# Kernel optimization log

Hardware: AMD Instinct MI355X
Metric: run time of the kernel (lower is better)

Reference implementation:

```python
import jax, jax.numpy as jnp
import numpy as np

CHEB_K = 3  # from init_kwargs

def _layernorm(v, g, b, eps=1e-12):
    mu = jnp.mean(v, axis=-1, keepdims=True)
    var = jnp.var(v, axis=-1, keepdims=True)  # biased, matches torch LayerNorm
    return (v - mu) * jax.lax.rsqrt(var + eps) * g + b

def setup_inputs() -> dict:
    key = jax.random.key(0)
    ks = jax.random.split(key, 5)
    B, N, D_IN, D_OUT, E = 64, 2048, 64, 64, 16
    return {
        "x": jax.random.normal(ks[0], (B, N, D_IN), dtype=jnp.float32),
        "node_embeddings": jax.random.normal(ks[1], (N, E), dtype=jnp.float32),
        "time_embeddings": jax.random.normal(ks[2], (E,), dtype=jnp.float32),
        "weights_pool": jax.random.normal(ks[3], (E, CHEB_K, D_IN, D_OUT), dtype=jnp.float32) * 0.1,
        "bias_pool": jax.random.normal(ks[4], (E, D_OUT), dtype=jnp.float32) * 0.1,
        "ln_gamma": jnp.ones((E,), dtype=jnp.float32),
        "ln_beta": jnp.zeros((E,), dtype=jnp.float32),
    }

def reference(x, node_embeddings, time_embeddings, weights_pool, bias_pool, ln_gamma, ln_beta):
    N = node_embeddings.shape[0]
    # dropout in eval mode -> identity
    ne = _layernorm(node_embeddings + time_embeddings[None, :], ln_gamma, ln_beta)  # [N,E]
    supports0 = jax.nn.softmax(ne @ ne.T, axis=1)  # [N,N]
    support_set = [jnp.eye(N, dtype=x.dtype), supports0]
    for _ in range(2, CHEB_K):
        support_set.append(2.0 * supports0 @ support_set[-1] - support_set[-2])
    supports = jnp.stack(support_set, axis=0)  # [K,N,N]
    weights = jnp.einsum('nd,dkio->nkio', ne, weights_pool)  # [N,K,I,O]
    bias = ne @ bias_pool  # [N,O]
    x_g = jnp.einsum('knm,bmc->bnkc', supports, x)  # [B,N,K,I]
    return jnp.einsum('bnki,nkio->bno', x_g, weights) + bias  # [B,N,O]
```

## Files before the change

### kernel.cpp

```cpp
#include <hip/hip_runtime.h>
#include <stdint.h>

typedef unsigned short u16;
typedef __attribute__((ext_vector_type(8))) short   bf16x8;
typedef __attribute__((ext_vector_type(4))) float   f32x4;
typedef __attribute__((ext_vector_type(4))) u16     u16x4;
typedef __attribute__((ext_vector_type(8))) u16     u16x8;

#define NN 2048
#define BB 64
#define DD 64
#define XSTRIDE (NN*DD)

__device__ __forceinline__ float bf2f(u16 u) {
    union { unsigned int i; float f; } v; v.i = ((unsigned int)u) << 16; return v.f;
}
__device__ __forceinline__ u16 f2bf(float f) {
    union { float f; unsigned int i; } v; v.f = f;
    unsigned int u = v.i;
    return (u16)((u + 0x7fffu + ((u >> 16) & 1u)) >> 16);
}

typedef __attribute__((address_space(3))) unsigned int lds_u32_t;
typedef const __attribute__((address_space(1))) unsigned int g_u32_t;
__device__ __forceinline__ void gload_lds16(const void* g, void* l) {
    __builtin_amdgcn_global_load_lds((g_u32_t*)(uintptr_t)g, (lds_u32_t*)(uintptr_t)l, 16, 0, 0);
}

__global__ __launch_bounds__(256) void k_ln(const float* __restrict__ nodee,
                                            const float* __restrict__ timee,
                                            const float* __restrict__ gamma,
                                            const float* __restrict__ beta,
                                            float* __restrict__ ne,
                                            u16* __restrict__ neb) {
    int n = blockIdx.x * 256 + threadIdx.x;
    float v[16]; float mu = 0.f;
    const float4* p = (const float4*)(nodee + (long)n * 16);
#pragma unroll
    for (int i = 0; i < 4; i++) {
        float4 q = p[i];
        v[i*4+0]=q.x; v[i*4+1]=q.y; v[i*4+2]=q.z; v[i*4+3]=q.w;
    }
#pragma unroll
    for (int e = 0; e < 16; e++) { v[e] += timee[e]; mu += v[e]; }
    mu *= (1.f/16.f);
    float var = 0.f;
#pragma unroll
    for (int e = 0; e < 16; e++) { float d = v[e]-mu; var += d*d; }
    var *= (1.f/16.f);
    float rs = rsqrtf(var + 1e-12f);
    float4* o = (float4*)(ne + (long)n * 16);
    u16x8 nb[2];
#pragma unroll
    for (int i = 0; i < 4; i++) {
        float4 q;
        q.x = (v[i*4+0]-mu)*rs*gamma[i*4+0] + beta[i*4+0];
        q.y = (v[i*4+1]-mu)*rs*gamma[i*4+1] + beta[i*4+1];
        q.z = (v[i*4+2]-mu)*rs*gamma[i*4+2] + beta[i*4+2];
        q.w = (v[i*4+3]-mu)*rs*gamma[i*4+3] + beta[i*4+3];
        o[i] = q;
        nb[i>>1][(i&1)*4+0] = f2bf(q.x); nb[i>>1][(i&1)*4+1] = f2bf(q.y);
        nb[i>>1][(i&1)*4+2] = f2bf(q.z); nb[i>>1][(i&1)*4+3] = f2bf(q.w);
    }
    u16x8 z;
#pragma unroll
    for (int j = 0; j < 8; j++) z[j] = 0;
    u16x8* ob = (u16x8*)&neb[(long)n * 32];
    ob[0] = nb[0]; ob[1] = nb[1]; ob[2] = z; ob[3] = z;
}

__global__ __launch_bounds__(256) void k_wperm(const float* __restrict__ wp,
                                               u16* __restrict__ wpP) {
    int j = blockIdx.x * 256 + threadIdx.x;
    int o = j / 192, ki = j - o * 192;
    int src = ki * 64 + o;
    u16x8 ov[4];
#pragma unroll
    for (int e = 0; e < 16; e++) ov[e>>3][e&7] = f2bf(wp[(long)e*12288 + src]);
#pragma unroll
    for (int e = 0; e < 8; e++) { ov[2][e] = 0; ov[3][e] = 0; }
    u16x8* dst = (u16x8*)&wpP[(long)j * 32];
    dst[0]=ov[0]; dst[1]=ov[1]; dst[2]=ov[2]; dst[3]=ov[3];
}

__global__ __launch_bounds__(256) void k_softmax(const float* __restrict__ ne,
                                                 u16* __restrict__ S) {
    __shared__ float row[2048];
    __shared__ float red[8];
    int n = blockIdx.x, t = threadIdx.x;
    int wave = t >> 6, lane = t & 63;
    f32x4 nev[4];
#pragma unroll
    for (int i = 0; i < 4; i++) nev[i] = *(const f32x4*)&ne[n*16 + i*4];
    float lmax = -1e30f;
    for (int m = t; m < 2048; m += 256) {
        const f32x4* p = (const f32x4*)&ne[m*16];
        f32x4 d4 = nev[0]*p[0] + nev[1]*p[1] + nev[2]*p[2] + nev[3]*p[3];
        float d = d4[0]+d4[1]+d4[2]+d4[3];
        row[m] = d;
        lmax = fmaxf(lmax, d);
    }
#pragma unroll
    for (int off = 32; off > 0; off >>= 1) lmax = fmaxf(lmax, __shfl_xor(lmax, off));
    if (lane == 0) red[wave] = lmax;
    __syncthreads();
    float gmax = fmaxf(fmaxf(red[0], red[1]), fmaxf(red[2], red[3]));
    float lsum = 0.f;
    for (int m = t; m < 2048; m += 256) {
        float ev = __expf(row[m] - gmax);
        row[m] = ev;
        lsum += ev;
    }
#pragma unroll
    for (int off = 32; off > 0; off >>= 1) lsum += __shfl_xor(lsum, off);
    __syncthreads();
    if (lane == 0) red[wave] = lsum;
    __syncthreads();
    float inv = 1.f / (red[0]+red[1]+red[2]+red[3]);
    for (int m = t; m < 2048; m += 256)
        S[(long)n*2048 + m] = f2bf(row[m] * inv);
}

__global__ __launch_bounds__(256) void k_permute(const float* __restrict__ x,
                                                 u16* __restrict__ Xpt) {
    __shared__ u16 T[64][72];
    int bid = blockIdx.x;
    int b = bid >> 5, m0 = (bid & 31) * 64;
    int t = threadIdx.x;
#pragma unroll
    for (int it = 0; it < 4; it++) {
        int fi = it*256 + t;
        int row = fi >> 4, c4 = (fi & 15) * 4;
        float4 v = *(const float4*)&x[(long)b*XSTRIDE + (m0+row)*64 + c4];
        T[c4+0][row] = f2bf(v.x); T[c4+1][row] = f2bf(v.y);
        T[c4+2][row] = f2bf(v.z); T[c4+3][row] = f2bf(v.w);
    }
    __syncthreads();
#pragma unroll
    for (int it = 0; it < 2; it++) {
        int ch = it*256 + t;
        int c = ch >> 3, m8 = (ch & 7) * 8;
        u16x8 v = *(const u16x8*)&T[c][m8];
        *(u16x8*)&Xpt[(long)(b*64 + c)*2048 + m0 + m8] = v;
    }
}

__global__ __launch_bounds__(256) void k_gemm_bt(const u16* __restrict__ A,
                                                 const u16* __restrict__ Bt,
                                                 u16* __restrict__ C,
                                                 int M, int Ncols, int K) {
    __shared__ __align__(16) u16 As[128*32];
    __shared__ __align__(16) u16 Bs[128*32];
    const int t = threadIdx.x;
    const int wave = t >> 6, lane = t & 63;
    const int l15 = lane & 15, lhi = lane >> 4;
    const int m0 = blockIdx.y * 128;
    const int n0 = blockIdx.x * 128;
    const int wr = wave >> 1, wc = wave & 1;
    f32x4 acc[4][4] = {};
    const int srow = t >> 2;
    const int sk = (t & 3) * 8;
    const u16* gA = A + (long)(m0 + srow) * K + sk;
    const u16* gB = Bt + (long)(n0 + srow) * K + sk;
    const long half = (long)64 * K;
    u16* lA = As + wave * 512;
    u16* lB = Bs + wave * 512;
    const int aoff = (wr*64 + l15)*32 + lhi*8;
    const int boff = (wc*64 + l15)*32 + lhi*8;
    for (int k0 = 0; k0 < K; k0 += 32) {
        gload_lds16(gA + k0,        lA);
        gload_lds16(gA + k0 + half, lA + 2048);
        gload_lds16(gB + k0,        lB);
        gload_lds16(gB + k0 + half, lB + 2048);
        __syncthreads();
        bf16x8 af[4], bv[4];
#pragma unroll
        for (int m = 0; m < 4; m++) af[m] = *(const bf16x8*)&As[aoff + m*512];
#pragma unroll
        for (int q = 0; q < 4; q++) bv[q] = *(const bf16x8*)&Bs[boff + q*512];
#pragma unroll
        for (int m = 0; m < 4; m++)
#pragma unroll
            for (int q = 0; q < 4; q++)
                acc[m][q] = __builtin_amdgcn_mfma_f32_16x16x32_bf16(af[m], bv[q], acc[m][q], 0, 0, 0);
        __syncthreads();
    }
#pragma unroll
    for (int m = 0; m < 4; m++) {
        int row = m0 + wr*64 + m*16 + lhi*4;
#pragma unroll
        for (int q = 0; q < 4; q++) {
            int col = n0 + wc*64 + q*16 + l15;
#pragma unroll
            for (int r = 0; r < 4; r++)
                C[(long)(row + r) * Ncols + col] = f2bf(acc[m][q][r]);
        }
    }
}

__global__ __launch_bounds__(512, 2) void k_gemm_big(const u16* __restrict__ A,
                                                     const u16* __restrict__ Bt,
                                                     u16* __restrict__ C,
                                                     u16* __restrict__ Ct,
                                                     int M, int Ncols, int K) {
    __shared__ __align__(16) u16 LB[73728];
    const int t = threadIdx.x;
    const int wave = t >> 6, lane = t & 63;
    const int l15 = lane & 15, lhi = lane >> 4;
    const int nwg = gridDim.x * gridDim.y;
    const int wgid = blockIdx.y * gridDim.x + blockIdx.x;
    const int swz = (wgid & 7) * (nwg >> 3) + (wgid >> 3);
    const int by = swz / gridDim.x, bx = swz - by * gridDim.x;
    const int m0 = by * 128, n0 = bx * 256;
    const int wr = wave >> 2, wc = wave & 3;
    const int NT = K >> 6;
    f32x4 acc[4][4] = {};

    const int srow = t >> 3;
    const int sswz = ((t & 7) ^ (srow & 7)) * 8;
    const u16* gA0 = A  + (long)(m0 + srow) * K + sswz;
    const u16* gB0 = Bt + (long)(n0 + srow) * K + sswz;
    const long rP = (long)64 * K;
    const int ldsW = wave * 512;

    int curA = 0,     nxtA = 8192,  tgtA = 16384;
    int curB = 24576, nxtB = 40960, tgtB = 57344;

    gload_lds16(gA0,           &LB[curA + 0*4096 + ldsW]);
    gload_lds16(gA0 + rP,      &LB[curA + 1*4096 + ldsW]);
#pragma unroll
    for (int r = 0; r < 4; r++) gload_lds16(gB0 + r*rP,      &LB[curB + r*4096 + ldsW]);
    gload_lds16(gA0 + 64,      &LB[nxtA + 0*4096 + ldsW]);
    gload_lds16(gA0 + rP + 64, &LB[nxtA + 1*4096 + ldsW]);
#pragma unroll
    for (int r = 0; r < 4; r++) gload_lds16(gB0 + r*rP + 64, &LB[nxtB + r*4096 + ldsW]);
    asm volatile("s_waitcnt vmcnt(6)" ::: "memory");
    __builtin_amdgcn_s_barrier();
    asm volatile("" ::: "memory");

    const int rsw = l15 & 7;
    const int sw0 = (lhi ^ rsw) * 8;
    const int sw1 = ((4 + lhi) ^ rsw) * 8;
    const int abase = (wr*64 + l15) * 64;
    const int bbase = (wc*64 + l15) * 64;

#pragma unroll 1
    for (int tt = 0; tt < NT; tt++) {
        const bool stg = (tt + 2 < NT);
        const long ko2 = (long)((tt + 2) << 6);
        bf16x8 af0[4], af1[4], bv0[4], bv1[4];
#pragma unroll
        for (int m = 0; m < 4; m++) af0[m] = *(const bf16x8*)&LB[curA + abase + m*1024 + sw0];
        bv0[0] = *(const bf16x8*)&LB[curB + bbase + 0*1024 + sw0];
        bv0[1] = *(const bf16x8*)&LB[curB + bbase + 1*1024 + sw0];
        if (stg) {
            gload_lds16(gA0 + ko2,      &LB[tgtA + 0*4096 + ldsW]);
            gload_lds16(gA0 + rP + ko2, &LB[tgtA + 1*4096 + ldsW]);
        }
        __builtin_amdgcn_s_barrier();
        asm volatile("s_waitcnt lgkmcnt(0)" ::: "memory");
        __builtin_amdgcn_s_setprio(1);
#pragma unroll
        for (int m = 0; m < 4; m++)
#pragma unroll
            for (int q = 0; q < 2; q++)
                acc[m][q] = __builtin_amdgcn_mfma_f32_16x16x32_bf16(af0[m], bv0[q], acc[m][q], 0, 0, 0);
        __builtin_amdgcn_s_setprio(0);
        __builtin_amdgcn_s_barrier();
        bv0[2] = *(const bf16x8*)&LB[curB + bbase + 2*1024 + sw0];
        bv0[3] = *(const bf16x8*)&LB[curB + bbase + 3*1024 + sw0];
        if (stg) {
            gload_lds16(gB0 + ko2,      &LB[tgtB + 0*4096 + ldsW]);
            gload_lds16(gB0 + rP + ko2, &LB[tgtB + 1*4096 + ldsW]);
        }
        __builtin_amdgcn_s_barrier();
        asm volatile("s_waitcnt lgkmcnt(0)" ::: "memory");
        __builtin_amdgcn_s_setprio(1);
#pragma unroll
        for (int m = 0; m < 4; m++)
#pragma unroll
            for (int q = 2; q < 4; q++)
                acc[m][q] = __builtin_amdgcn_mfma_f32_16x16x32_bf16(af0[m], bv0[q], acc[m][q], 0, 0, 0);
        __builtin_amdgcn_s_setprio(0);
        __builtin_amdgcn_s_barrier();
#pragma unroll
        for (int m = 0; m < 4; m++) af1[m] = *(const bf16x8*)&LB[curA + abase + m*1024 + sw1];
        bv1[0] = *(const bf16x8*)&LB[curB + bbase + 0*1024 + sw1];
        bv1[1] = *(const bf16x8*)&LB[curB + bbase + 1*1024 + sw1];
        if (stg) {
            gload_lds16(gB0 + 2*rP + ko2, &LB[tgtB + 2*4096 + ldsW]);
            gload_lds16(gB0 + 3*rP + ko2, &LB[tgtB + 3*4096 + ldsW]);
        }
        __builtin_amdgcn_s_barrier();
        asm volatile("s_waitcnt lgkmcnt(0)" ::: "memory");
        __builtin_amdgcn_s_setprio(1);
#pragma unroll
        for (int m = 0; m < 4; m++)
#pragma unroll
            for (int q = 0; q < 2; q++)
                acc[m][q] = __builtin_amdgcn_mfma_f32_16x16x32_bf16(af1[m], bv1[q], acc[m][q], 0, 0, 0);
        __builtin_amdgcn_s_setprio(0);
        __builtin_amdgcn_s_barrier();
        bv1[2] = *(const bf16x8*)&LB[curB + bbase + 2*1024 + sw1];
        bv1[3] = *(const bf16x8*)&LB[curB + bbase + 3*1024 + sw1];
        __builtin_amdgcn_s_barrier();
        asm volatile("s_waitcnt lgkmcnt(0)" ::: "memory");
        __builtin_amdgcn_s_setprio(1);
#pragma unroll
        for (int m = 0; m < 4; m++)
#pragma unroll
            for (int q = 2; q < 4; q++)
                acc[m][q] = __builtin_amdgcn_mfma_f32_16x16x32_bf16(af1[m], bv1[q], acc[m][q], 0, 0, 0);
        __builtin_amdgcn_s_setprio(0);
        asm volatile("" ::: "memory");
        if (tt + 1 < NT) {
            if (stg) asm volatile("s_waitcnt vmcnt(6)" ::: "memory");
            else     asm volatile("s_waitcnt vmcnt(0)" ::: "memory");
            __builtin_amdgcn_s_barrier();
            asm volatile("" ::: "memory");
        }
        int ta = curA; curA = nxtA; nxtA = tgtA; tgtA = ta;
        int tb = curB; curB = nxtB; nxtB = tgtB; tgtB = tb;
    }
#pragma unroll
    for (int m = 0; m < 4; m++) {
        int row = m0 + wr*64 + m*16 + lhi*4;
#pragma unroll
        for (int q = 0; q < 4; q++) {
            int col = n0 + wc*64 + q*16 + l15;
#pragma unroll
            for (int r = 0; r < 4; r++)
                C[(long)(row + r) * Ncols + col] = f2bf(acc[m][q][r]);
        }
    }
    if (Ct != nullptr) {
        __syncthreads();
#pragma unroll
        for (int m = 0; m < 4; m++) {
            int rowb = wr*64 + m*16 + lhi*4;
#pragma unroll
            for (int q = 0; q < 4; q++) {
                int col = wc*64 + q*16 + l15;
                u16x4 p;
                p[0]=f2bf(acc[m][q][0]); p[1]=f2bf(acc[m][q][1]);
                p[2]=f2bf(acc[m][q][2]); p[3]=f2bf(acc[m][q][3]);
                *(u16x4*)&LB[col*136 + rowb] = p;
            }
        }
        __syncthreads();
        const int j16 = t >> 4, ch = (t & 15) * 8;
#pragma unroll
        for (int p = 0; p < 8; p++) {
            int j = p*32 + j16;
            u16x8 v = *(const u16x8*)&LB[j*136 + ch];
            *(u16x8*)&Ct[(long)(n0 + j)*M + m0 + ch] = v;
        }
    }
}

__global__ __launch_bounds__(256) void k_final(const float* __restrict__ x,
                                               const u16* __restrict__ Y1,
                                               const u16* __restrict__ Y2,
                                               const u16* __restrict__ Wt,
                                               const float* __restrict__ ne,
                                               const float* __restrict__ bp,
                                               float* __restrict__ out) {
    __shared__ __align__(16) u16 Al[64*200];
    __shared__ __align__(16) u16 Wl[64*200];
    __shared__ float biasl[64];
    int n = blockIdx.x;
    int t = threadIdx.x;
    int wave = t >> 6, lane = t & 63;
    int l15 = lane & 15, lhi = lane >> 4;
#pragma unroll
    for (int it = 0; it < 6; it++) {
        int ch = it*256 + t;
        int o = ch / 24, kl = (ch % 24) * 8;
        u16x8 v = *(const u16x8*)&Wt[(long)n*12288 + ch*8];
        *(u16x8*)&Wl[o*200 + kl] = v;
    }
    float xs[16];
#pragma unroll
    for (int it = 0; it < 4; it++) {
        int fi = it*256 + t;
        int b = fi >> 4, i4 = (fi & 15) * 4;
        float4 v = *(const float4*)&x[(long)b*XSTRIDE + n*64 + i4];
        xs[it*4+0]=v.x; xs[it*4+1]=v.y; xs[it*4+2]=v.z; xs[it*4+3]=v.w;
        u16x4 p; p[0]=f2bf(v.x); p[1]=f2bf(v.y); p[2]=f2bf(v.z); p[3]=f2bf(v.w);
        *(u16x4*)&Al[b*200 + i4] = p;
    }
#pragma unroll
    for (int it = 0; it < 2; it++) {
        int ch = it*256 + t;
        int b = ch >> 3, i8 = (ch & 7)*8;
        u16x8 v = *(const u16x8*)&Y1[(long)n*4096 + ch*8];
        *(u16x8*)&Al[b*200 + 64 + i8] = v;
    }
#pragma unroll
    for (int it = 0; it < 4; it++) {
        int fi = it*256 + t;
        int b = fi >> 4, i4 = (fi & 15)*4;
        u16x4 y = *(const u16x4*)&Y2[(long)n*4096 + fi*4];
        u16x4 p;
#pragma unroll
        for (int j = 0; j < 4; j++) p[j] = f2bf(2.f*bf2f(y[j]) - xs[it*4+j]);
        *(u16x4*)&Al[b*200 + 128 + i4] = p;
    }
    if (t < 64) {
        float s = 0.f;
#pragma unroll
        for (int e = 0; e < 16; e++) s += ne[n*16+e] * bp[e*64 + t];
        biasl[t] = s;
    }
    __syncthreads();
    f32x4 acc[4] = {};
#pragma unroll
    for (int kk = 0; kk < 6; kk++) {
        bf16x8 bv = *(const bf16x8*)&Wl[(wave*16 + l15)*200 + kk*32 + lhi*8];
#pragma unroll
        for (int m = 0; m < 4; m++) {
            bf16x8 av = *(const bf16x8*)&Al[(m*16 + l15)*200 + kk*32 + lhi*8];
            acc[m] = __builtin_amdgcn_mfma_f32_16x16x32_bf16(av, bv, acc[m], 0, 0, 0);
        }
    }
    int o = wave*16 + l15;
    float bias = biasl[o];
#pragma unroll
    for (int m = 0; m < 4; m++) {
        int brow = m*16 + lhi*4;
#pragma unroll
        for (int r = 0; r < 4; r++)
            out[(long)(brow + r)*XSTRIDE + n*64 + o] = acc[m][r] + bias;
    }
}

extern "C" void kernel_launch(void* const* d_in, const int* in_sizes, int n_in,
                              void* d_out, int out_size, void* d_ws, size_t ws_size,
                              hipStream_t stream) {
    const float* x     = (const float*)d_in[0];
    const float* nodee = (const float*)d_in[1];
    const float* timee = (const float*)d_in[2];
    const float* wp    = (const float*)d_in[3];
    const float* bp    = (const float*)d_in[4];
    const float* gamma = (const float*)d_in[5];
    const float* beta  = (const float*)d_in[6];
    float* out = (float*)d_out;

    char* ws = (char*)d_ws;
    float* ne  = (float*)(ws);
    u16* S     = (u16*)(ws + 131072);
    u16* Xpt   = (u16*)(ws + 8519680);
    u16* Y1    = (u16*)(ws + 25296896);
    u16* Y1t   = (u16*)(ws + 42074112);
    u16* Y2    = (u16*)(ws + 58851328);
    u16* Wt    = (u16*)(ws + 75628544);
    u16* neb   = (u16*)(ws + 58851328);
    u16* wpP   = (u16*)(ws + 58851328 + 131072);
    if (ws_size < (size_t)125960192) return;

    k_ln      <<<8,    256, 0, stream>>>(nodee, timee, gamma, beta, ne, neb);
    k_wperm   <<<48,   256, 0, stream>>>(wp, wpP);
    k_gemm_bt <<<dim3(96,16), 256, 0, stream>>>(neb, wpP, Wt, 2048, 12288, 32);
    k_softmax <<<2048, 256, 0, stream>>>(ne, S);
    k_permute <<<2048, 256, 0, stream>>>(x, Xpt);
    k_gemm_big<<<dim3(16,16), 512, 0, stream>>>(S, Xpt, Y1, Y1t, 2048, 4096, 2048);
    k_gemm_big<<<dim3(16,16), 512, 0, stream>>>(S, Y1t, Y2, (u16*)nullptr, 2048, 4096, 2048);
    k_final   <<<2048, 256, 0, stream>>>(x, Y1, Y2, Wt, ne, bp, out);
}
```

Baseline: 155.9 us.

## Drop intra-iteration barriers in big GEMM loop and lower occupancy target

Replaces the four-phase ping-pong schedule inside the big GEMM main loop (with barriers between each MFMA cluster) with two half-K phases that issue all LDS fragment loads and then 16 MFMAs, leaving a single barrier per iteration. Global-to-LDS prefetch issue is redistributed across the two halves. Launch bounds drop from 2 to 1 workgroups per CU, allowing more registers per thread but reducing cross-workgroup latency hiding. The intent is to cut barrier stalls, at the cost of occupancy and of less interleaving between LDS reads and MFMA.

Result: faster. 150.7 us (-3.4%).

```diff
diff --git a/kernel.cpp b/kernel.cpp
--- a/kernel.cpp
+++ b/kernel.cpp
@@ -198,7 +198,7 @@
     }
 }
 
-__global__ __launch_bounds__(512, 2) void k_gemm_big(const u16* __restrict__ A,
+__global__ __launch_bounds__(512, 1) void k_gemm_big(const u16* __restrict__ A,
                                                      const u16* __restrict__ Bt,
                                                      u16* __restrict__ C,
                                                      u16* __restrict__ Ct,
@@ -248,74 +248,48 @@
     for (int tt = 0; tt < NT; tt++) {
         const bool stg = (tt + 2 < NT);
         const long ko2 = (long)((tt + 2) << 6);
-        bf16x8 af0[4], af1[4], bv0[4], bv1[4];
-#pragma unroll
-        for (int m = 0; m < 4; m++) af0[m] = *(const bf16x8*)&LB[curA + abase + m*1024 + sw0];
-        bv0[0] = *(const bf16x8*)&LB[curB + bbase + 0*1024 + sw0];
-        bv0[1] = *(const bf16x8*)&LB[curB + bbase + 1*1024 + sw0];
-        if (stg) {
-            gload_lds16(gA0 + ko2,      &LB[tgtA + 0*4096 + ldsW]);
-            gload_lds16(gA0 + rP + ko2, &LB[tgtA + 1*4096 + ldsW]);
-        }
-        __builtin_amdgcn_s_barrier();
-        asm volatile("s_waitcnt lgkmcnt(0)" ::: "memory");
-        __builtin_amdgcn_s_setprio(1);
-#pragma unroll
-        for (int m = 0; m < 4; m++)
-#pragma unroll
-            for (int q = 0; q < 2; q++)
-                acc[m][q] = __builtin_amdgcn_mfma_f32_16x16x32_bf16(af0[m], bv0[q], acc[m][q], 0, 0, 0);
-        __builtin_amdgcn_s_setprio(0);
-        __builtin_amdgcn_s_barrier();
-        bv0[2] = *(const bf16x8*)&LB[curB + bbase + 2*1024 + sw0];
-        bv0[3] = *(const bf16x8*)&LB[curB + bbase + 3*1024 + sw0];
-        if (stg) {
-            gload_lds16(gB0 + ko2,      &LB[tgtB + 0*4096 + ldsW]);
-            gload_lds16(gB0 + rP + ko2, &LB[tgtB + 1*4096 + ldsW]);
-        }
-        __builtin_amdgcn_s_barrier();
-        asm volatile("s_waitcnt lgkmcnt(0)" ::: "memory");
-        __builtin_amdgcn_s_setprio(1);
-#pragma unroll
-        for (int m = 0; m < 4; m++)
-#pragma unroll
-            for (int q = 2; q < 4; q++)
-                acc[m][q] = __builtin_amdgcn_mfma_f32_16x16x32_bf16(af0[m], bv0[q], acc[m][q], 0, 0, 0);
-        __builtin_amdgcn_s_setprio(0);
-        __builtin_amdgcn_s_barrier();
-#pragma unroll
-        for (int m = 0; m < 4; m++) af1[m] = *(const bf16x8*)&LB[curA + abase + m*1024 + sw1];
-        bv1[0] = *(const bf16x8*)&LB[curB + bbase + 0*1024 + sw1];
-        bv1[1] = *(const bf16x8*)&LB[curB + bbase + 1*1024 + sw1];
-        if (stg) {
-            gload_lds16(gB0 + 2*rP + ko2, &LB[tgtB + 2*4096 + ldsW]);
-            gload_lds16(gB0 + 3*rP + ko2, &LB[tgtB + 3*4096 + ldsW]);
-        }
-        __builtin_amdgcn_s_barrier();
-        asm volatile("s_waitcnt lgkmcnt(0)" ::: "memory");
-        __builtin_amdgcn_s_setprio(1);
-#pragma unroll
-        for (int m = 0; m < 4; m++)
-#pragma unroll
-            for (int q = 0; q < 2; q++)
-                acc[m][q] = __builtin_amdgcn_mfma_f32_16x16x32_bf16(af1[m], bv1[q], acc[m][q], 0, 0, 0);
-        __builtin_amdgcn_s_setprio(0);
-        __builtin_amdgcn_s_barrier();
-        bv1[2] = *(const bf16x8*)&LB[curB + bbase + 2*1024 + sw1];
-        bv1[3] = *(const bf16x8*)&LB[curB + bbase + 3*1024 + sw1];
-        __builtin_amdgcn_s_barrier();
-        asm volatile("s_waitcnt lgkmcnt(0)" ::: "memory");
-        __builtin_amdgcn_s_setprio(1);
-#pragma unroll
-        for (int m = 0; m < 4; m++)
-#pragma unroll
-            for (int q = 2; q < 4; q++)
-                acc[m][q] = __builtin_amdgcn_mfma_f32_16x16x32_bf16(af1[m], bv1[q], acc[m][q], 0, 0, 0);
-        __builtin_amdgcn_s_setprio(0);
+        {
+            bf16x8 af[4], bv[4];
+#pragma unroll
+            for (int m = 0; m < 4; m++) af[m] = *(const bf16x8*)&LB[curA + abase + m*1024 + sw0];
+#pragma unroll
+            for (int q = 0; q < 4; q++) bv[q] = *(const bf16x8*)&LB[curB + bbase + q*1024 + sw0];
+            if (stg) {
+                gload_lds16(gA0 + ko2,      &LB[tgtA + 0*4096 + ldsW]);
+                gload_lds16(gA0 + rP + ko2, &LB[tgtA + 1*4096 + ldsW]);
+                gload_lds16(gB0 + ko2,      &LB[tgtB + 0*4096 + ldsW]);
+            }
+            __builtin_amdgcn_s_setprio(1);
+#pragma unroll
+            for (int m = 0; m < 4; m++)
+#pragma unroll
+                for (int q = 0; q < 4; q++)
+                    acc[m][q] = __builtin_amdgcn_mfma_f32_16x16x32_bf16(af[m], bv[q], acc[m][q], 0, 0, 0);
+            __builtin_amdgcn_s_setprio(0);
+        }
+        {
+            bf16x8 af[4], bv[4];
+#pragma unroll
+            for (int m = 0; m < 4; m++) af[m] = *(const bf16x8*)&LB[curA + abase + m*1024 + sw1];
+#pragma unroll
+            for (int q = 0; q < 4; q++) bv[q] = *(const bf16x8*)&LB[curB + bbase + q*1024 + sw1];
+            if (stg) {
+                gload_lds16(gB0 + 1*rP + ko2, &LB[tgtB + 1*4096 + ldsW]);
+                gload_lds16(gB0 + 2*rP + ko2, &LB[tgtB + 2*4096 + ldsW]);
+                gload_lds16(gB0 + 3*rP + ko2, &LB[tgtB + 3*4096 + ldsW]);
+            }
+            __builtin_amdgcn_s_setprio(1);
+#pragma unroll
+            for (int m = 0; m < 4; m++)
+#pragma unroll
+                for (int q = 0; q < 4; q++)
+                    acc[m][q] = __builtin_amdgcn_mfma_f32_16x16x32_bf16(af[m], bv[q], acc[m][q], 0, 0, 0);
+            __builtin_amdgcn_s_setprio(0);
+        }
         asm volatile("" ::: "memory");
+        if (stg)                asm volatile("s_waitcnt vmcnt(6)" ::: "memory");
+        else if (tt + 1 < NT)   asm volatile("s_waitcnt vmcnt(0)" ::: "memory");
         if (tt + 1 < NT) {
-            if (stg) asm volatile("s_waitcnt vmcnt(6)" ::: "memory");
-            else     asm volatile("s_waitcnt vmcnt(0)" ::: "memory");
             __builtin_amdgcn_s_barrier();
             asm volatile("" ::: "memory");
         }
```
